# Kernel optimization log

Hardware: AMD Instinct MI355X
Metric: run time of the kernel (lower is better)

The kernel has to match this reference:

```python
import jax, jax.numpy as jnp
import numpy as np

D_MODEL = 1024
N_HEAD = 16
B, S = 4, 1024


def setup_inputs() -> dict:
    key = jax.random.key(0)
    ks = jax.random.split(key, 10)
    f = lambda k, shp: jax.random.normal(k, shp, dtype=jnp.float32)
    return {
        "x": f(ks[0], (B, S, D_MODEL)),
        "y": f(ks[1], (B, S, D_MODEL)),
        "z": f(ks[2], (B, S, D_MODEL)),
        "mask": f(ks[3], (1, 1, S, S)) * 0.1,
        "wq_w": f(ks[4], (D_MODEL, D_MODEL)) * (D_MODEL ** -0.5),
        "wq_b": f(ks[5], (D_MODEL,)) * 0.02,
        "wk_w": f(ks[6], (D_MODEL, D_MODEL)) * (D_MODEL ** -0.5),
        "wk_b": f(ks[7], (D_MODEL,)) * 0.02,
        "wv_w": f(ks[8], (D_MODEL, D_MODEL)) * (D_MODEL ** -0.5),
        "wv_b": f(ks[9], (D_MODEL,)) * 0.02,
    }


def reference(x, y, z, mask, wq_w, wq_b, wk_w, wk_b, wv_w, wv_b):
    b, xl, d = x.shape
    hd = d // N_HEAD
    # linear projections (torch Linear: x @ W^T + b)
    q = x @ wq_w.T + wq_b
    k = y @ wk_w.T + wk_b
    v = z @ wv_w.T + wv_b
    # [B, H, L, hd]
    q = q.reshape(b, xl, N_HEAD, hd).transpose(0, 2, 1, 3)
    k = k.reshape(b, y.shape[1], N_HEAD, hd).transpose(0, 2, 1, 3)
    v = v.reshape(b, z.shape[1], N_HEAD, hd).transpose(0, 2, 1, 3)
    # NOTE: source scales by sqrt(d_model), not sqrt(head_dim)
    scale = 1.0 / jnp.sqrt(jnp.asarray(d, dtype=x.dtype))
    logits = jnp.einsum("bhqd,bhkd->bhqk", q, k) * scale
    score = jax.nn.softmax(logits, axis=-1)
    # mask added AFTER softmax (faithful to source)
    score = score + mask
    out = jnp.einsum("bhqk,bhkd->bhqd", score, v)
    return out.transpose(0, 2, 1, 3).reshape(b, xl, d)
```

## Files before the change

### kernel.cpp

```cpp
#include <hip/hip_runtime.h>
#include <hip/hip_bf16.h>
#include <cstdint>

typedef __bf16 bf16_t;
typedef __bf16 bf16x8 __attribute__((ext_vector_type(8)));
typedef __bf16 bf16x4 __attribute__((ext_vector_type(4)));
typedef float floatx4 __attribute__((ext_vector_type(4)));

typedef __attribute__((address_space(3))) uint32_t lds_u32_t;
typedef const __attribute__((address_space(1))) uint32_t g_u32_t;

#define MFMA_BF16(a, b, c) __builtin_amdgcn_mfma_f32_16x16x32_bf16((a), (b), (c), 0, 0, 0)

#if __has_builtin(__builtin_amdgcn_exp2f)
#define EXP2F(x) __builtin_amdgcn_exp2f(x)
#else
#define EXP2F(x) __expf((x) * 0.6931471805599453f)
#endif

static constexpr int S = 1024;
static constexpr int HD = 64;

struct ConvArgs {
  const float* src[7];
  bf16_t* dst[7];
  int n[7];
};

__global__ __launch_bounds__(256) void convert_kernel(ConvArgs a) {
  const int j = blockIdx.y;
  const float4* __restrict__ s = (const float4*)a.src[j];
  bf16x8* __restrict__ d = (bf16x8*)a.dst[j];
  const int n8 = a.n[j] >> 3;
  for (int i = blockIdx.x * blockDim.x + threadIdx.x; i < n8; i += gridDim.x * blockDim.x) {
    float4 v0 = s[2 * i];
    float4 v1 = s[2 * i + 1];
    bf16x8 o;
    o[0] = (bf16_t)v0.x; o[1] = (bf16_t)v0.y; o[2] = (bf16_t)v0.z; o[3] = (bf16_t)v0.w;
    o[4] = (bf16_t)v1.x; o[5] = (bf16_t)v1.y; o[6] = (bf16_t)v1.z; o[7] = (bf16_t)v1.w;
    d[i] = o;
  }
}

struct GemmCfg {
  const bf16_t* A;
  const bf16_t* Bm;
  void* out;
  const float* bias;
  int mode;
  float scale;
};

union GemmSmem {
  struct { bf16_t A[128 * 64]; bf16_t B[128 * 64]; } ab;
  bf16_t C[128 * 136];
};

__global__ __launch_bounds__(256, 3) void gemm_nt_kernel(GemmCfg c0, GemmCfg c1, GemmCfg c2, int K) {
  GemmCfg cfg = (blockIdx.y == 0) ? c0 : (blockIdx.y == 1 ? c1 : c2);
  __shared__ GemmSmem u;
  __shared__ float bias_s[128];
  const int tid = threadIdx.x;
  const int wave = tid >> 6;
  const int lane = tid & 63;
  const int g = lane >> 4;
  const int cl = lane & 15;
  const int mq = (wave & 1) * 64;
  const int nq = (wave >> 1) * 64;

  const int xcd = blockIdx.x & 7, idx = blockIdx.x >> 3;
  int mb, nb;
  if (cfg.mode == 0) { mb = xcd * 4 + (idx & 3); nb = idx >> 2; }
  else               { nb = xcd * 4 + (idx & 3); mb = idx >> 2; }
  const int m0 = mb * 128, n0 = nb * 128;

  if (tid < 128) bias_s[tid] = cfg.bias[(cfg.mode == 0 ? n0 : m0) + tid];

  const int srow = tid >> 3;
  const int sch = (tid & 7) ^ (srow & 7);
  const bf16_t* Ag = cfg.A + (size_t)(m0 + srow) * K + sch * 8;
  const bf16_t* Bg = cfg.Bm + (size_t)(n0 + srow) * K + sch * 8;
  const int swz = cl & 7;

  floatx4 acc[4][4];
#pragma unroll
  for (int i = 0; i < 4; ++i)
#pragma unroll
    for (int j = 0; j < 4; ++j) acc[i][j] = floatx4{0.f, 0.f, 0.f, 0.f};

  const int kiters = K >> 6;
  for (int kt = 0; kt < kiters; ++kt) {
    __syncthreads();
#pragma unroll
    for (int i = 0; i < 4; ++i) {
      __builtin_amdgcn_global_load_lds((g_u32_t*)(const void*)(Ag + (size_t)(i * 32) * K),
                                       (lds_u32_t*)(void*)&u.ab.A[(i * 256 + tid) * 8], 16, 0, 0);
      __builtin_amdgcn_global_load_lds((g_u32_t*)(const void*)(Bg + (size_t)(i * 32) * K),
                                       (lds_u32_t*)(void*)&u.ab.B[(i * 256 + tid) * 8], 16, 0, 0);
    }
    Ag += 64;
    Bg += 64;
    __syncthreads();

#pragma unroll
    for (int kc = 0; kc < 2; ++kc) {
      bf16x8 af[4], bfr[4];
#pragma unroll
      for (int i = 0; i < 4; ++i)
        af[i] = *(const bf16x8*)&u.ab.A[(mq + i * 16 + cl) * 64 + ((kc * 4 + g) ^ swz) * 8];
#pragma unroll
      for (int j = 0; j < 4; ++j)
        bfr[j] = *(const bf16x8*)&u.ab.B[(nq + j * 16 + cl) * 64 + ((kc * 4 + g) ^ swz) * 8];
#pragma unroll
      for (int i = 0; i < 4; ++i)
#pragma unroll
        for (int j = 0; j < 4; ++j) acc[i][j] = MFMA_BF16(af[i], bfr[j], acc[i][j]);
    }
  }

  __syncthreads();
#pragma unroll
  for (int i = 0; i < 4; ++i)
#pragma unroll
    for (int j = 0; j < 4; ++j)
#pragma unroll
      for (int r = 0; r < 4; ++r) {
        const int ml = mq + i * 16 + g * 4 + r;
        const int nl = nq + j * 16 + cl;
        float v = (acc[i][j][r] + bias_s[cfg.mode == 0 ? nl : ml]) * cfg.scale;
        u.C[ml * 136 + nl] = (bf16_t)v;
      }
  __syncthreads();
#pragma unroll
  for (int it = 0; it < 8; ++it) {
    const int ix = it * 256 + tid;
    const int ml = ix >> 4, nc = ix & 15;
    bf16x8 val = *(const bf16x8*)&u.C[ml * 136 + nc * 8];
    const int m = m0 + ml, n = n0 + nc * 8;
    size_t addr;
    if (cfg.mode == 0)
      addr = (size_t)((m >> 10) * 16 + (n >> 6)) * 65536 + (m & 1023) * 64 + (n & 63);
    else
      addr = (size_t)((n >> 10) * 16 + (m >> 6)) * 65536 + (m & 63) * 1024 + (n & 1023);
    *(bf16x8*)&((bf16_t*)cfg.out)[addr] = val;
  }
}

__global__ __launch_bounds__(256, 2) void attn_kernel(const bf16_t* __restrict__ Q,
                                                      const bf16_t* __restrict__ Kb,
                                                      const bf16_t* __restrict__ Vt,
                                                      const bf16_t* __restrict__ Mk,
                                                      float* __restrict__ out) {
  __shared__ bf16_t Ks[128 * 64];
  __shared__ bf16_t Vs[64 * 128];
  __shared__ bf16_t Pbuf[4][32 * 136];
  const int tid = threadIdx.x;
  const int wave = tid >> 6, lane = tid & 63;
  const int g = lane >> 4, cl = lane & 15;
  const int bh = blockIdx.x & 63, qt = blockIdx.x >> 6;
  const int q0w = qt * 128 + wave * 32;
  const bf16_t* Qp = Q + (size_t)bh * (S * HD);
  const bf16_t* Kp = Kb + (size_t)bh * (S * HD);
  const bf16_t* Vp = Vt + (size_t)bh * (S * HD);
  bf16_t* Pw = &Pbuf[wave][0];

  const int krow = tid >> 3, kch = (tid & 7) ^ (krow & 7);
  const int vrow = tid >> 4, vch = (tid & 15) ^ (vrow & 7);
  const int sw = cl & 7;

  bf16x8 qf[2][2];
#pragma unroll
  for (int nj = 0; nj < 2; ++nj)
#pragma unroll
    for (int kc = 0; kc < 2; ++kc)
      qf[nj][kc] = *(const bf16x8*)&Qp[(size_t)(q0w + nj * 16 + cl) * HD + kc * 32 + g * 8];

  floatx4 o[2][4], o2[2][4];
#pragma unroll
  for (int mi = 0; mi < 2; ++mi)
#pragma unroll
    for (int nj = 0; nj < 4; ++nj) {
      o[mi][nj] = floatx4{0.f, 0.f, 0.f, 0.f};
      o2[mi][nj] = floatx4{0.f, 0.f, 0.f, 0.f};
    }
  float dsq[2] = {0.f, 0.f};

  for (int kt = 0; kt < 8; ++kt) {
    const int k0 = kt * 128;
    __syncthreads();
#pragma unroll
    for (int i = 0; i < 4; ++i)
      __builtin_amdgcn_global_load_lds(
          (g_u32_t*)(const void*)&Kp[(size_t)(k0 + i * 32 + krow) * HD + kch * 8],
          (lds_u32_t*)(void*)&Ks[(i * 256 + tid) * 8], 16, 0, 0);
#pragma unroll
    for (int i = 0; i < 4; ++i)
      __builtin_amdgcn_global_load_lds(
          (g_u32_t*)(const void*)&Vp[(size_t)(i * 16 + vrow) * S + k0 + vch * 8],
          (lds_u32_t*)(void*)&Vs[(i * 256 + tid) * 8], 16, 0, 0);

    bf16x8 ma0[4], ma1[4];
#pragma unroll
    for (int kc = 0; kc < 4; ++kc) {
      ma0[kc] = *(const bf16x8*)&Mk[(size_t)(q0w + cl) * S + k0 + kc * 32 + g * 8];
      ma1[kc] = *(const bf16x8*)&Mk[(size_t)(q0w + 16 + cl) * S + k0 + kc * 32 + g * 8];
    }
    __syncthreads();

#pragma unroll
    for (int mi = 0; mi < 8; ++mi) {
      bf16x8 kf0 = *(const bf16x8*)&Ks[(mi * 16 + cl) * 64 + ((0 + g) ^ sw) * 8];
      bf16x8 kf1 = *(const bf16x8*)&Ks[(mi * 16 + cl) * 64 + ((4 + g) ^ sw) * 8];
      floatx4 s0 = floatx4{0.f, 0.f, 0.f, 0.f}, s1 = floatx4{0.f, 0.f, 0.f, 0.f};
      s0 = MFMA_BF16(kf0, qf[0][0], s0);
      s0 = MFMA_BF16(kf1, qf[0][1], s0);
      s1 = MFMA_BF16(kf0, qf[1][0], s1);
      s1 = MFMA_BF16(kf1, qf[1][1], s1);
      bf16x4 p0, p1;
#pragma unroll
      for (int r = 0; r < 4; ++r) {
        float e0 = EXP2F(s0[r]);
        float e1 = EXP2F(s1[r]);
        dsq[0] += e0;
        dsq[1] += e1;
        p0[r] = (bf16_t)e0;
        p1[r] = (bf16_t)e1;
      }
      *(bf16x4*)&Pw[(cl)*136 + mi * 16 + g * 4] = p0;
      *(bf16x4*)&Pw[(16 + cl) * 136 + mi * 16 + g * 4] = p1;
    }

#pragma unroll
    for (int kc = 0; kc < 4; ++kc) {
      bf16x8 pa0 = *(const bf16x8*)&Pw[cl * 136 + kc * 32 + g * 8];
      bf16x8 pa1 = *(const bf16x8*)&Pw[(16 + cl) * 136 + kc * 32 + g * 8];
#pragma unroll
      for (int nj = 0; nj < 4; ++nj) {
        bf16x8 vf = *(const bf16x8*)&Vs[(nj * 16 + cl) * 128 + ((kc * 4 + g) ^ sw) * 8];
        o[0][nj] = MFMA_BF16(pa0, vf, o[0][nj]);
        o[1][nj] = MFMA_BF16(pa1, vf, o[1][nj]);
        o2[0][nj] = MFMA_BF16(ma0[kc], vf, o2[0][nj]);
        o2[1][nj] = MFMA_BF16(ma1[kc], vf, o2[1][nj]);
      }
    }
  }

#pragma unroll
  for (int nj = 0; nj < 2; ++nj) {
    dsq[nj] += __shfl_xor(dsq[nj], 16, 64);
    dsq[nj] += __shfl_xor(dsq[nj], 32, 64);
  }

  const int b = bh >> 4, h = bh & 15;
#pragma unroll
  for (int mi = 0; mi < 2; ++mi) {
#pragma unroll
    for (int r = 0; r < 4; ++r) {
      float dv = __shfl(dsq[mi], g * 4 + r, 64);
      float dinv = 1.0f / dv;
      const int srow = q0w + mi * 16 + g * 4 + r;
#pragma unroll
      for (int nj = 0; nj < 4; ++nj) {
        const int hd = nj * 16 + cl;
        out[((size_t)b * S + srow) * 1024 + h * HD + hd] = o[mi][nj][r] * dinv + o2[mi][nj][r];
      }
    }
  }
}

extern "C" void kernel_launch(void* const* d_in, const int* in_sizes, int n_in,
                              void* d_out, int out_size, void* d_ws, size_t ws_size,
                              hipStream_t stream) {
  const float* x = (const float*)d_in[0];
  const float* y = (const float*)d_in[1];
  const float* z = (const float*)d_in[2];
  const float* mask = (const float*)d_in[3];
  const float* wq_w = (const float*)d_in[4];
  const float* wq_b = (const float*)d_in[5];
  const float* wk_w = (const float*)d_in[6];
  const float* wk_b = (const float*)d_in[7];
  const float* wv_w = (const float*)d_in[8];
  const float* wv_b = (const float*)d_in[9];

  uint8_t* ws = (uint8_t*)d_ws;
  const size_t MB = 1u << 20;
  bf16_t* Xb = (bf16_t*)(ws + 0 * MB);
  bf16_t* Yb = (bf16_t*)(ws + 8 * MB);
  bf16_t* Zb = (bf16_t*)(ws + 16 * MB);
  bf16_t* Wqb = (bf16_t*)(ws + 24 * MB);
  bf16_t* Wkb = (bf16_t*)(ws + 26 * MB);
  bf16_t* Wvb = (bf16_t*)(ws + 28 * MB);
  bf16_t* Mb = (bf16_t*)(ws + 30 * MB);
  bf16_t* Qb = (bf16_t*)(ws + 32 * MB);
  bf16_t* Kb = (bf16_t*)(ws + 40 * MB);
  bf16_t* Vtb = (bf16_t*)(ws + 48 * MB);

  ConvArgs ca;
  ca.src[0] = x;    ca.dst[0] = Xb;  ca.n[0] = 4 * 1024 * 1024;
  ca.src[1] = y;    ca.dst[1] = Yb;  ca.n[1] = 4 * 1024 * 1024;
  ca.src[2] = z;    ca.dst[2] = Zb;  ca.n[2] = 4 * 1024 * 1024;
  ca.src[3] = wq_w; ca.dst[3] = Wqb; ca.n[3] = 1024 * 1024;
  ca.src[4] = wk_w; ca.dst[4] = Wkb; ca.n[4] = 1024 * 1024;
  ca.src[5] = wv_w; ca.dst[5] = Wvb; ca.n[5] = 1024 * 1024;
  ca.src[6] = mask; ca.dst[6] = Mb;  ca.n[6] = 1024 * 1024;
  convert_kernel<<<dim3(512, 7), 256, 0, stream>>>(ca);

  const float qscale = 0.0450842200277801f;
  GemmCfg cq{Xb, Wqb, (void*)Qb, wq_b, 0, qscale};
  GemmCfg ck{Yb, Wkb, (void*)Kb, wk_b, 0, 1.0f};
  GemmCfg cv{Wvb, Zb, (void*)Vtb, wv_b, 1, 1.0f};
  gemm_nt_kernel<<<dim3(256, 3), 256, 0, stream>>>(cq, ck, cv, 1024);

  attn_kernel<<<dim3(512), 256, 0, stream>>>(Qb, Kb, Vtb, Mb, (float*)d_out);
}
```

Before: 184.0 us.

## Rewrite attention with 32x32 MFMA, register-resident P via permlane swap, no LDS

Switches the attention kernel from 16x16x32 to 32x32x16 MFMA tiles. K, V and mask fragments now load directly from global memory into registers instead of being staged through LDS, which removes the shared buffers and the block barriers. The softmax probabilities are repacked in registers with v_permlane32_swap instead of a round trip through LDS, and the denominator reduction uses a single shuffle plus bpermute. The cost is more global or L2 traffic, since each wave loads K and V itself without sharing across the block, and higher register pressure.

```diff
diff --git a/kernel.cpp b/kernel.cpp
--- a/kernel.cpp
+++ b/kernel.cpp
@@ -6,11 +6,14 @@
 typedef __bf16 bf16x8 __attribute__((ext_vector_type(8)));
 typedef __bf16 bf16x4 __attribute__((ext_vector_type(4)));
 typedef float floatx4 __attribute__((ext_vector_type(4)));
+typedef float floatx16 __attribute__((ext_vector_type(16)));
+typedef uint32_t u32x4 __attribute__((ext_vector_type(4)));
 
 typedef __attribute__((address_space(3))) uint32_t lds_u32_t;
 typedef const __attribute__((address_space(1))) uint32_t g_u32_t;
 
 #define MFMA_BF16(a, b, c) __builtin_amdgcn_mfma_f32_16x16x32_bf16((a), (b), (c), 0, 0, 0)
+#define MFMA32_BF16(a, b, c) __builtin_amdgcn_mfma_f32_32x32x16_bf16((a), (b), (c), 0, 0, 0)
 
 #if __has_builtin(__builtin_amdgcn_exp2f)
 #define EXP2F(x) __builtin_amdgcn_exp2f(x)
@@ -151,120 +154,121 @@
                                                       const bf16_t* __restrict__ Vt,
                                                       const bf16_t* __restrict__ Mk,
                                                       float* __restrict__ out) {
-  __shared__ bf16_t Ks[128 * 64];
-  __shared__ bf16_t Vs[64 * 128];
-  __shared__ bf16_t Pbuf[4][32 * 136];
   const int tid = threadIdx.x;
   const int wave = tid >> 6, lane = tid & 63;
-  const int g = lane >> 4, cl = lane & 15;
+  const int l31 = lane & 31, hi = lane >> 5;
   const int bh = blockIdx.x & 63, qt = blockIdx.x >> 6;
   const int q0w = qt * 128 + wave * 32;
   const bf16_t* Qp = Q + (size_t)bh * (S * HD);
   const bf16_t* Kp = Kb + (size_t)bh * (S * HD);
   const bf16_t* Vp = Vt + (size_t)bh * (S * HD);
-  bf16_t* Pw = &Pbuf[wave][0];
-
-  const int krow = tid >> 3, kch = (tid & 7) ^ (krow & 7);
-  const int vrow = tid >> 4, vch = (tid & 15) ^ (vrow & 7);
-  const int sw = cl & 7;
-
-  bf16x8 qf[2][2];
-#pragma unroll
-  for (int nj = 0; nj < 2; ++nj)
-#pragma unroll
-    for (int kc = 0; kc < 2; ++kc)
-      qf[nj][kc] = *(const bf16x8*)&Qp[(size_t)(q0w + nj * 16 + cl) * HD + kc * 32 + g * 8];
-
-  floatx4 o[2][4], o2[2][4];
-#pragma unroll
-  for (int mi = 0; mi < 2; ++mi)
-#pragma unroll
-    for (int nj = 0; nj < 4; ++nj) {
-      o[mi][nj] = floatx4{0.f, 0.f, 0.f, 0.f};
-      o2[mi][nj] = floatx4{0.f, 0.f, 0.f, 0.f};
-    }
-  float dsq[2] = {0.f, 0.f};
+  const bf16_t* Mp = Mk + (size_t)(q0w + l31) * S;
+
+  bf16x8 qf[4];
+#pragma unroll
+  for (int kk = 0; kk < 4; ++kk)
+    qf[kk] = *(const bf16x8*)&Qp[(size_t)(q0w + l31) * HD + kk * 16 + hi * 8];
+
+  floatx16 o[2], o2[2];
+#pragma unroll
+  for (int nt = 0; nt < 2; ++nt) {
+#pragma unroll
+    for (int r = 0; r < 16; ++r) { o[nt][r] = 0.f; o2[nt][r] = 0.f; }
+  }
+  float dsq = 0.f;
 
   for (int kt = 0; kt < 8; ++kt) {
     const int k0 = kt * 128;
-    __syncthreads();
-#pragma unroll
-    for (int i = 0; i < 4; ++i)
-      __builtin_amdgcn_global_load_lds(
-          (g_u32_t*)(const void*)&Kp[(size_t)(k0 + i * 32 + krow) * HD + kch * 8],
-          (lds_u32_t*)(void*)&Ks[(i * 256 + tid) * 8], 16, 0, 0);
-#pragma unroll
-    for (int i = 0; i < 4; ++i)
-      __builtin_amdgcn_global_load_lds(
-          (g_u32_t*)(const void*)&Vp[(size_t)(i * 16 + vrow) * S + k0 + vch * 8],
-          (lds_u32_t*)(void*)&Vs[(i * 256 + tid) * 8], 16, 0, 0);
-
-    bf16x8 ma0[4], ma1[4];
+
+    bf16x8 kf[4][4];
+#pragma unroll
+    for (int mt = 0; mt < 4; ++mt)
+#pragma unroll
+      for (int kk = 0; kk < 4; ++kk)
+        kf[mt][kk] = *(const bf16x8*)&Kp[(size_t)(k0 + mt * 32 + l31) * HD + kk * 16 + hi * 8];
+
+    floatx16 s[4];
+#pragma unroll
+    for (int mt = 0; mt < 4; ++mt) {
+#pragma unroll
+      for (int r = 0; r < 16; ++r) s[mt][r] = 0.f;
+#pragma unroll
+      for (int kk = 0; kk < 4; ++kk) s[mt] = MFMA32_BF16(kf[mt][kk], qf[kk], s[mt]);
+    }
+
+    bf16x8 vfA[2][4], mfA[4];
 #pragma unroll
     for (int kc = 0; kc < 4; ++kc) {
-      ma0[kc] = *(const bf16x8*)&Mk[(size_t)(q0w + cl) * S + k0 + kc * 32 + g * 8];
-      ma1[kc] = *(const bf16x8*)&Mk[(size_t)(q0w + 16 + cl) * S + k0 + kc * 32 + g * 8];
-    }
-    __syncthreads();
-
-#pragma unroll
-    for (int mi = 0; mi < 8; ++mi) {
-      bf16x8 kf0 = *(const bf16x8*)&Ks[(mi * 16 + cl) * 64 + ((0 + g) ^ sw) * 8];
-      bf16x8 kf1 = *(const bf16x8*)&Ks[(mi * 16 + cl) * 64 + ((4 + g) ^ sw) * 8];
-      floatx4 s0 = floatx4{0.f, 0.f, 0.f, 0.f}, s1 = floatx4{0.f, 0.f, 0.f, 0.f};
-      s0 = MFMA_BF16(kf0, qf[0][0], s0);
-      s0 = MFMA_BF16(kf1, qf[0][1], s0);
-      s1 = MFMA_BF16(kf0, qf[1][0], s1);
-      s1 = MFMA_BF16(kf1, qf[1][1], s1);
-      bf16x4 p0, p1;
-#pragma unroll
-      for (int r = 0; r < 4; ++r) {
-        float e0 = EXP2F(s0[r]);
-        float e1 = EXP2F(s1[r]);
-        dsq[0] += e0;
-        dsq[1] += e1;
-        p0[r] = (bf16_t)e0;
-        p1[r] = (bf16_t)e1;
-      }
-      *(bf16x4*)&Pw[(cl)*136 + mi * 16 + g * 4] = p0;
-      *(bf16x4*)&Pw[(16 + cl) * 136 + mi * 16 + g * 4] = p1;
-    }
-
+#pragma unroll
+      for (int nt = 0; nt < 2; ++nt)
+        vfA[nt][kc] = *(const bf16x8*)&Vp[(size_t)(nt * 32 + l31) * S + k0 + kc * 16 + hi * 8];
+      mfA[kc] = *(const bf16x8*)&Mp[k0 + kc * 16 + hi * 8];
+    }
+
+    bf16x8 pf[8];
+#pragma unroll
+    for (int mt = 0; mt < 4; ++mt) {
+      float e[16];
+#pragma unroll
+      for (int r = 0; r < 16; ++r) {
+        e[r] = EXP2F(s[mt][r]);
+        dsq += e[r];
+      }
+      uint32_t c[8];
+#pragma unroll
+      for (int i = 0; i < 8; ++i) {
+        bf16_t lo = (bf16_t)e[2 * i], hh = (bf16_t)e[2 * i + 1];
+        c[i] = (uint32_t)__builtin_bit_cast(uint16_t, lo) |
+               ((uint32_t)__builtin_bit_cast(uint16_t, hh) << 16);
+      }
+      asm volatile("v_permlane32_swap_b32 %0, %1" : "+v"(c[0]), "+v"(c[2]));
+      asm volatile("v_permlane32_swap_b32 %0, %1" : "+v"(c[1]), "+v"(c[3]));
+      asm volatile("v_permlane32_swap_b32 %0, %1" : "+v"(c[4]), "+v"(c[6]));
+      asm volatile("v_permlane32_swap_b32 %0, %1" : "+v"(c[5]), "+v"(c[7]));
+      u32x4 pe = {c[0], c[1], c[2], c[3]};
+      u32x4 po = {c[4], c[5], c[6], c[7]};
+      pf[2 * mt] = __builtin_bit_cast(bf16x8, pe);
+      pf[2 * mt + 1] = __builtin_bit_cast(bf16x8, po);
+    }
+
+    bf16x8 vfB[2][4], mfB[4];
 #pragma unroll
     for (int kc = 0; kc < 4; ++kc) {
-      bf16x8 pa0 = *(const bf16x8*)&Pw[cl * 136 + kc * 32 + g * 8];
-      bf16x8 pa1 = *(const bf16x8*)&Pw[(16 + cl) * 136 + kc * 32 + g * 8];
-#pragma unroll
-      for (int nj = 0; nj < 4; ++nj) {
-        bf16x8 vf = *(const bf16x8*)&Vs[(nj * 16 + cl) * 128 + ((kc * 4 + g) ^ sw) * 8];
-        o[0][nj] = MFMA_BF16(pa0, vf, o[0][nj]);
-        o[1][nj] = MFMA_BF16(pa1, vf, o[1][nj]);
-        o2[0][nj] = MFMA_BF16(ma0[kc], vf, o2[0][nj]);
-        o2[1][nj] = MFMA_BF16(ma1[kc], vf, o2[1][nj]);
-      }
-    }
-  }
-
-#pragma unroll
-  for (int nj = 0; nj < 2; ++nj) {
-    dsq[nj] += __shfl_xor(dsq[nj], 16, 64);
-    dsq[nj] += __shfl_xor(dsq[nj], 32, 64);
-  }
+#pragma unroll
+      for (int nt = 0; nt < 2; ++nt)
+        vfB[nt][kc] = *(const bf16x8*)&Vp[(size_t)(nt * 32 + l31) * S + k0 + (kc + 4) * 16 + hi * 8];
+      mfB[kc] = *(const bf16x8*)&Mp[k0 + (kc + 4) * 16 + hi * 8];
+    }
+
+#pragma unroll
+    for (int kc = 0; kc < 4; ++kc)
+#pragma unroll
+      for (int nt = 0; nt < 2; ++nt) {
+        o[nt] = MFMA32_BF16(pf[kc], vfA[nt][kc], o[nt]);
+        o2[nt] = MFMA32_BF16(mfA[kc], vfA[nt][kc], o2[nt]);
+      }
+#pragma unroll
+    for (int kc = 0; kc < 4; ++kc)
+#pragma unroll
+      for (int nt = 0; nt < 2; ++nt) {
+        o[nt] = MFMA32_BF16(pf[kc + 4], vfB[nt][kc], o[nt]);
+        o2[nt] = MFMA32_BF16(mfB[kc], vfB[nt][kc], o2[nt]);
+      }
+  }
+
+  dsq += __shfl_xor(dsq, 32, 64);
+  float dinv = 1.0f / dsq;
 
   const int b = bh >> 4, h = bh & 15;
 #pragma unroll
-  for (int mi = 0; mi < 2; ++mi) {
-#pragma unroll
-    for (int r = 0; r < 4; ++r) {
-      float dv = __shfl(dsq[mi], g * 4 + r, 64);
-      float dinv = 1.0f / dv;
-      const int srow = q0w + mi * 16 + g * 4 + r;
-#pragma unroll
-      for (int nj = 0; nj < 4; ++nj) {
-        const int hd = nj * 16 + cl;
-        out[((size_t)b * S + srow) * 1024 + h * HD + hd] = o[mi][nj][r] * dinv + o2[mi][nj][r];
-      }
-    }
+  for (int r = 0; r < 16; ++r) {
+    const int qr = (r & 3) + 8 * (r >> 2) + 4 * hi;
+    float dv = __builtin_bit_cast(
+        float, __builtin_amdgcn_ds_bpermute(qr << 2, __builtin_bit_cast(int, dinv)));
+    const int srow = q0w + qr;
+#pragma unroll
+    for (int nt = 0; nt < 2; ++nt)
+      out[((size_t)b * S + srow) * 1024 + h * HD + nt * 32 + l31] = o[nt][r] * dv + o2[nt][r];
   }
 }
 
```

After: 226.2 us. 22.9% more time.
